# Performance work log

Measured on AMD Instinct MI355X. Metric: run time of the kernel, lower is better.

## Reference

```python
import jax, jax.numpy as jnp
import numpy as np

N_NODES = 100000
N_EDGES = 1600000
IN_DIM = 128
HID = 128
OUT_DIM = 64
EPS = 1e-8


def setup_inputs() -> dict:
    key = jax.random.key(0)
    ks = jax.random.split(key, 10)
    x = jax.random.normal(ks[0], (N_NODES, IN_DIM), dtype=jnp.float32)
    edge_index = jax.random.randint(ks[1], (2, N_EDGES), 0, N_NODES, dtype=jnp.int64)
    edge_attr = jax.random.uniform(ks[2], (N_EDGES, 4), dtype=jnp.float32)
    s1 = 1.0 / np.sqrt(IN_DIM)
    s2 = 1.0 / np.sqrt(HID)
    sr = 1.0 / np.sqrt(2 * HID)
    W1 = jax.random.normal(ks[3], (HID, IN_DIM), dtype=jnp.float32) * s1
    b1 = jnp.zeros((HID,), dtype=jnp.float32)
    W2 = jax.random.normal(ks[4], (HID, HID), dtype=jnp.float32) * s2
    b2 = jnp.zeros((HID,), dtype=jnp.float32)
    Wr = jax.random.normal(ks[5], (OUT_DIM, 2 * HID), dtype=jnp.float32) * sr
    br = jnp.zeros((OUT_DIM,), dtype=jnp.float32)
    return {"x": x, "edge_index": edge_index, "edge_attr": edge_attr,
            "W1": W1, "b1": b1, "W2": W2, "b2": b2, "Wr": Wr, "br": br}


def _edge_weight_from_attr_auto(edge_attr):
    # mean over features, min-max normalize, invert, clamp >= 0
    m = edge_attr.mean(axis=-1)                      # [E]
    m_min, m_max = m.min(), m.max()
    m_norm = (m - m_min) / (m_max - m_min + EPS)
    w = jnp.where(m_max - m_min > EPS, 1.0 - m_norm, jnp.ones_like(m))
    return jnp.clip(w, 0.0)


def reference(x, edge_index, edge_attr, W1, b1, W2, b2, Wr, br):
    N = x.shape[0]
    row, col = edge_index[0], edge_index[1]          # source -> target
    ew = _edge_weight_from_attr_auto(edge_attr)      # [E]
    # GCN normalization with self-loops (self-loop weight = 1.0)
    deg = jax.ops.segment_sum(ew, col, num_segments=N) + 1.0   # [N]
    dis = jax.lax.rsqrt(deg)                         # deg >= 1
    norm = dis[row] * ew * dis[col]                  # [E]

    def gcn(h, W, b):
        hW = h @ W.T                                 # [N, d_out]
        agg = jax.ops.segment_sum(norm[:, None] * hW[row], col, num_segments=N)
        # self-loop contribution: dis[i] * 1.0 * dis[i] * hW[i]
        return agg + (dis * dis)[:, None] * hW + b

    # dropout in eval mode -> identity
    h1 = jax.nn.relu(gcn(x, W1, b1))                 # [N, HID]
    h2 = jax.nn.relu(gcn(h1, W2, b2))                # [N, HID]
    hcat = jnp.concatenate([h1, h2], axis=-1)        # [N, 2*HID] (JK concat)
    return hcat @ Wr.T + br                          # residue-level [N, OUT_DIM]
```

## Files before the change

kernel.cpp:

```cpp
#include <hip/hip_runtime.h>

#define NN 100000
#define NE 1600000
#define HID 128
#define ODIM 64
#define NBK 196
#define BSHIFT 9
#define BGRID 800
#define CVTB 32
#define GEMMB 3125
#define CHUNK 2000
#define BITER 8
#define BINCAP 12288
#define SMAX 2588
#define LMAX 647

typedef unsigned int u32;
typedef unsigned short u16;
typedef __bf16 bf16x8 __attribute__((ext_vector_type(8)));
typedef float f32x4 __attribute__((ext_vector_type(4)));
typedef float f32x2 __attribute__((ext_vector_type(2)));

__device__ __forceinline__ float bf_lo(u32 p){ return __uint_as_float(p << 16); }
__device__ __forceinline__ float bf_hi(u32 p){ return __uint_as_float(p & 0xffff0000u); }
__device__ __forceinline__ u16 f2bf(float f){
  u32 u = __float_as_uint(f);
  u += 0x7fffu + ((u >> 16) & 1u);
  return (u16)(u >> 16);
}
__device__ __forceinline__ bf16x8 ld8bf(const u16* p){ return *(const bf16x8*)p; }
__device__ __forceinline__ bf16x8 cvt8(const float* p){
  union { bf16x8 v; u16 s[8]; } r;
#pragma unroll
  for (int i = 0; i < 8; i++) r.s[i] = f2bf(p[i]);
  return r.v;
}

__device__ __forceinline__ void wparams(const u32* minmax, float* A, float* B){
  u32 mnq = 32767u - minmax[0];
  u32 mxq = minmax[1];
  u32 rngq = mxq - mnq;
  float inv = rngq ? 1.f / ((float)rngq * (1.f / 32767.f) + 1e-8f) : 0.f;
  *A = 1.f + (float)mnq * (1.f / 32767.f) * inv;
  *B = inv * (1.f / 32767.f);
}

__global__ __launch_bounds__(256, 4) void k_front(
    const float* __restrict__ eattr, const int* __restrict__ erow,
    const int* __restrict__ ecol, u32* __restrict__ bcur,
    u32* __restrict__ binA, u16* __restrict__ binM, u32* __restrict__ minmax,
    const float* __restrict__ x, const float* __restrict__ W1,
    const float* __restrict__ W2, const float* __restrict__ Wr,
    u16* __restrict__ W2b, u16* __restrict__ Wrb, u16* __restrict__ graw){
  int tid = threadIdx.x;
  int bid = blockIdx.x;
  if (bid >= BGRID + CVTB){
    int gblk = bid - BGRID - CVTB;
    int wave = tid >> 6, lane = tid & 63;
    int m0 = gblk * 32;
    int m = lane & 15, q = lane >> 4;
    const float* a0f = x + (size_t)(m0 + m) * HID;
    const float* a1f = a0f + (size_t)16 * HID;
    const float* brow0 = W1 + (size_t)(wave * 16 + m) * HID;
    const float* brow1 = brow0 + (size_t)64 * HID;
    f32x4 acc00 = {0.f,0.f,0.f,0.f}, acc01 = {0.f,0.f,0.f,0.f};
    f32x4 acc10 = {0.f,0.f,0.f,0.f}, acc11 = {0.f,0.f,0.f,0.f};
#pragma unroll
    for (int kb = 0; kb < HID; kb += 32){
      bf16x8 af0 = cvt8(a0f + kb + q * 8);
      bf16x8 af1 = cvt8(a1f + kb + q * 8);
      bf16x8 bf0 = cvt8(brow0 + kb + q * 8);
      bf16x8 bf1 = cvt8(brow1 + kb + q * 8);
      acc00 = __builtin_amdgcn_mfma_f32_16x16x32_bf16(af0, bf0, acc00, 0, 0, 0);
      acc01 = __builtin_amdgcn_mfma_f32_16x16x32_bf16(af0, bf1, acc01, 0, 0, 0);
      acc10 = __builtin_amdgcn_mfma_f32_16x16x32_bf16(af1, bf0, acc10, 0, 0, 0);
      acc11 = __builtin_amdgcn_mfma_f32_16x16x32_bf16(af1, bf1, acc11, 0, 0, 0);
    }
    u16* crow0 = graw + (size_t)(m0 + q * 4) * HID + wave * 16 + m;
    u16* crow1 = crow0 + (size_t)16 * HID;
#pragma unroll
    for (int r = 0; r < 4; r++){
      crow0[(size_t)r * HID]      = f2bf(acc00[r]);
      crow0[(size_t)r * HID + 64] = f2bf(acc01[r]);
      crow1[(size_t)r * HID]      = f2bf(acc10[r]);
      crow1[(size_t)r * HID + 64] = f2bf(acc11[r]);
    }
    return;
  }
  if (bid >= BGRID){
    int i = (bid - BGRID) * 256 + tid;
    const float* src; u16* dst; int off;
    if (i < 4096){ src = W2; dst = W2b; off = i; }
    else { src = Wr; dst = Wrb; off = i - 4096; }
    float4 v = ((const float4*)src)[off];
    uint2 o;
    o.x = (u32)f2bf(v.x) | ((u32)f2bf(v.y) << 16);
    o.y = (u32)f2bf(v.z) | ((u32)f2bf(v.w) << 16);
    ((uint2*)dst)[off] = o;
    return;
  }
  __shared__ u32 lcnt4[4 * NBK], wof4[4 * NBK];
  __shared__ u32 lofs[NBK], gb[NBK];
  __shared__ u32 scn[256];
  __shared__ u16 lmap[LMAX];
  __shared__ u32 stageA[SMAX];
  __shared__ u16 stageM[SMAX];
  __shared__ u32 Tt;
  __shared__ u32 sMn[4], sMx[4];
  for (int t = tid; t < 4 * NBK; t += 256) lcnt4[t] = 0;
  __syncthreads();
  int base = bid * CHUNK;
  int wid = tid >> 6, lane = tid & 63;
  u32 lmn = 0, lmx = 0;
  u32 pk[BITER], sd[BITER], mq8[BITER];
#pragma unroll
  for (int it = 0; it < BITER; it++){
    int idx = it * 256 + tid;
    u32 p = 0xFFFFFFFFu, srcd = 0, mq = 0;
    if (idx < CHUNK){
      int e = base + idx;
      float4 a = ((const float4*)eattr)[e];
      float m = 0.25f * (a.x + a.y + a.z + a.w);
      mq = (u32)(m * 32767.f + 0.5f);
      lmn = max(lmn, 32767u - mq); lmx = max(lmx, mq);
      int c = ecol[e];
      u32 s = (u32)erow[e]; if (s >= NN) s = 0;
      if ((u32)c < NN){
        u32 b = (u32)c >> BSHIFT;
        u32 r = atomicAdd(&lcnt4[wid * NBK + b], 1u);
        p = (b << 21) | r;
        srcd = s | (((u32)c & 511u) << 17);
      }
    }
    pk[it] = p; sd[it] = srcd; mq8[it] = mq;
  }
  __syncthreads();
  u32 na = 0, n = 0;
  if (tid < NBK){
    u32 n0 = lcnt4[tid], n1 = lcnt4[NBK + tid];
    u32 n2 = lcnt4[2 * NBK + tid], n3 = lcnt4[3 * NBK + tid];
    n = n0 + n1 + n2 + n3;
    na = (n + 3u) & ~3u;
    wof4[tid] = 0; wof4[NBK + tid] = n0;
    wof4[2 * NBK + tid] = n0 + n1; wof4[3 * NBK + tid] = n0 + n1 + n2;
  }
  scn[tid] = na; __syncthreads();
  for (int s = 1; s < 256; s <<= 1){
    u32 t = (tid >= s) ? scn[tid - s] : 0;
    __syncthreads();
    scn[tid] += t;
    __syncthreads();
  }
  u32 ex = scn[tid] - na;
  if (tid < NBK){
    lofs[tid] = ex;
    u32 g = 0x80000000u;
    if (na){
      u32 gl = atomicAdd(&bcur[tid], na);
      if (gl + na <= BINCAP) g = (u32)tid * BINCAP + gl;
    }
    gb[tid] = g;
    for (u32 l = ex >> 2; l < (ex + na) >> 2; l++) lmap[l] = (u16)tid;
    for (u32 k = n; k < na; k++){ stageA[ex + k] = 0xFFFFFFFFu; stageM[ex + k] = 0; }
  }
  if (tid == 255) Tt = scn[255];
  __syncthreads();
#pragma unroll
  for (int it = 0; it < BITER; it++){
    u32 p = pk[it];
    if (p == 0xFFFFFFFFu) continue;
    u32 b = p >> 21;
    u32 slot = lofs[b] + wof4[wid * NBK + b] + (p & 4095u);
    stageA[slot] = sd[it];
    stageM[slot] = (u16)mq8[it];
  }
  __syncthreads();
  u32 T = Tt;
  for (u32 i = tid; i < T; i += 256){
    u32 b = lmap[i >> 2];
    u32 g = gb[b];
    if (g != 0x80000000u){
      u32 o = g + (i - lofs[b]);
      binA[o] = stageA[i];
      binM[o] = stageM[i];
    }
  }
  for (int off = 32; off; off >>= 1){
    lmn = max(lmn, (u32)__shfl_xor((int)lmn, off));
    lmx = max(lmx, (u32)__shfl_xor((int)lmx, off));
  }
  if (lane == 0){ sMn[wid] = lmn; sMx[wid] = lmx; }
  __syncthreads();
  if (tid == 0){
    u32 mn = max(max(sMn[0], sMn[1]), max(sMn[2], sMn[3]));
    u32 mx = max(max(sMx[0], sMx[1]), max(sMx[2], sMx[3]));
    atomicMax(&minmax[0], mn);
    atomicMax(&minmax[1], mx);
  }
}

__global__ __launch_bounds__(1024) void k_scatter(
    const u32* __restrict__ bcur, const u32* __restrict__ binA,
    const u16* __restrict__ binM, const u32* __restrict__ minmax,
    u32* __restrict__ csr, u32* __restrict__ meta, float* __restrict__ dis){
  __shared__ u32 cntL[512], sumL[512], curL[512];
  __shared__ u32 wtot[8];
  int b = blockIdx.x, tid = threadIdx.x;
  int bb = b * BINCAP;
  int nrec = (int)min(bcur[b], (u32)BINCAP);
  if (tid < 512){ cntL[tid] = 0; sumL[tid] = 0; }
  __syncthreads();
  for (int i = tid; i < nrec; i += 1024){
    u32 a = binA[bb + i];
    if (a == 0xFFFFFFFFu) continue;
    u32 d = (a >> 17) & 511u;
    u32 mq = binM[bb + i];
    atomicAdd(&cntL[d], 1u);
    atomicAdd(&sumL[d], mq);
  }
  __syncthreads();
  float A, B; wparams(minmax, &A, &B);
  int wid = tid >> 6, lane = tid & 63;
  u32 v = 0, incl = 0;
  if (tid < 512){ v = cntL[tid]; incl = v; }
  for (int off = 1; off < 64; off <<= 1){
    u32 t = (u32)__shfl_up((int)incl, off);
    if (lane >= off) incl += t;
  }
  if (tid < 512 && lane == 63) wtot[wid] = incl;
  __syncthreads();
  if (tid < 512){
    u32 pre = 0;
#pragma unroll
    for (int k = 0; k < 8; k++) pre += (k < wid) ? wtot[k] : 0u;
    u32 ex = pre + incl - v;
    curL[tid] = (u32)bb + ex;
    int node = (b << BSHIFT) + tid;
    if (node < NN){
      meta[node] = ((u32)bb + ex) | (v << 22);
      float sw = A * (float)v - B * (float)sumL[tid];
      dis[node] = rsqrtf(1.f + sw);
    }
  }
  __syncthreads();
  for (int i = tid; i < nrec; i += 1024){
    u32 a = binA[bb + i];
    if (a == 0xFFFFFFFFu) continue;
    u32 d = (a >> 17) & 511u;
    u32 mq = binM[bb + i];
    u32 pos = atomicAdd(&curL[d], 1u);
    csr[pos] = (a & 0x1FFFFu) | (mq << 17);
  }
}

__global__ __launch_bounds__(256) void k_gemm128(
    const u16* __restrict__ Ab, const u16* __restrict__ Bt,
    const float* __restrict__ dis, u16* __restrict__ G){
  int wave = threadIdx.x >> 6, lane = threadIdx.x & 63;
  int m0 = blockIdx.x * 32;
  int m = lane & 15, q = lane >> 4;
  const u16* a0b = Ab + (size_t)(m0 + m) * HID;
  const u16* a1b = a0b + (size_t)16 * HID;
  const u16* brow0 = Bt + (size_t)(wave * 16 + m) * HID;
  const u16* brow1 = brow0 + (size_t)64 * HID;
  f32x4 acc00 = {0.f,0.f,0.f,0.f}, acc01 = {0.f,0.f,0.f,0.f};
  f32x4 acc10 = {0.f,0.f,0.f,0.f}, acc11 = {0.f,0.f,0.f,0.f};
#pragma unroll
  for (int kb = 0; kb < HID; kb += 32){
    bf16x8 af0 = ld8bf(a0b + kb + q * 8);
    bf16x8 af1 = ld8bf(a1b + kb + q * 8);
    bf16x8 bf0 = ld8bf(brow0 + kb + q * 8);
    bf16x8 bf1 = ld8bf(brow1 + kb + q * 8);
    acc00 = __builtin_amdgcn_mfma_f32_16x16x32_bf16(af0, bf0, acc00, 0, 0, 0);
    acc01 = __builtin_amdgcn_mfma_f32_16x16x32_bf16(af0, bf1, acc01, 0, 0, 0);
    acc10 = __builtin_amdgcn_mfma_f32_16x16x32_bf16(af1, bf0, acc10, 0, 0, 0);
    acc11 = __builtin_amdgcn_mfma_f32_16x16x32_bf16(af1, bf1, acc11, 0, 0, 0);
  }
  u16* crow0 = G + (size_t)(m0 + q * 4) * HID + wave * 16 + m;
  u16* crow1 = crow0 + (size_t)16 * HID;
#pragma unroll
  for (int r = 0; r < 4; r++){
    float d0 = dis[m0 + q * 4 + r];
    float d1 = dis[m0 + 16 + q * 4 + r];
    crow0[(size_t)r * HID]      = f2bf(acc00[r] * d0);
    crow0[(size_t)r * HID + 64] = f2bf(acc01[r] * d0);
    crow1[(size_t)r * HID]      = f2bf(acc10[r] * d1);
    crow1[(size_t)r * HID + 64] = f2bf(acc11[r] * d1);
  }
}

template <bool FD>
__global__ __launch_bounds__(256) void k_aggregate(
    const u32* __restrict__ meta, const u32* __restrict__ csr,
    const float* __restrict__ dis, const u32* __restrict__ minmax,
    const u16* __restrict__ g, const float* __restrict__ bias,
    u16* __restrict__ hout){
  int node = __builtin_amdgcn_readfirstlane(
      (int)(blockIdx.x * 4 + (threadIdx.x >> 6)));
  int lane = threadIdx.x & 63;
  const u32* gp = (const u32*)g;
  u32 sv = gp[((size_t)node << 6) + lane];
  u32 mw = meta[node];
  float di = dis[node];
  float A, B; wparams(minmax, &A, &B);
  u32 s = mw & 0x3FFFFFu;
  int c = (int)(mw >> 22);
  const u32* cp = csr + s;
  f32x2 acc = {0.f, 0.f};
  int j = 0;
  for (; j + 16 <= c; j += 16){
    u32 p[16];
#pragma unroll
    for (int t = 0; t < 16; t++)
      p[t] = __builtin_amdgcn_readfirstlane(cp[j + t]);
    u32 pv[16];
#pragma unroll
    for (int t = 0; t < 16; t++)
      pv[t] = gp[(size_t)(p[t] & 0x1FFFFu) * 64u + lane];
#pragma unroll
    for (int t = 0; t < 16; t++){
      float wf = A - B * (float)(p[t] >> 17);
      if (FD) wf *= dis[p[t] & 0x1FFFFu];
      f32x2 val = {bf_lo(pv[t]), bf_hi(pv[t])};
      f32x2 w2 = {wf, wf};
      acc += w2 * val;
    }
  }
  for (; j < c; j += 8){
    u32 p[8];
#pragma unroll
    for (int t = 0; t < 8; t++)
      p[t] = __builtin_amdgcn_readfirstlane(cp[j + t]);
    u32 st[8]; float wv[8];
#pragma unroll
    for (int t = 0; t < 8; t++){
      bool ok = (j + t) < c;
      st[t] = ok ? (p[t] & 0x1FFFFu) : 0u;
      float wf = A - B * (float)(p[t] >> 17);
      if (FD) wf *= dis[st[t]];
      wv[t] = ok ? wf : 0.f;
    }
    u32 pv[8];
#pragma unroll
    for (int t = 0; t < 8; t++)
      pv[t] = gp[(size_t)st[t] * 64u + lane];
#pragma unroll
    for (int t = 0; t < 8; t++){
      f32x2 val = {bf_lo(pv[t]), bf_hi(pv[t])};
      f32x2 w2 = {wv[t], wv[t]};
      acc += w2 * val;
    }
  }
  float2 bv = ((const float2*)bias)[lane];
  f32x2 selfv = {bf_lo(sv), bf_hi(sv)};
  float sc = FD ? di : 1.f;
  float o0 = fmaxf((acc.x + sc * selfv.x) * di + bv.x, 0.f);
  float o1 = fmaxf((acc.y + sc * selfv.y) * di + bv.y, 0.f);
  ((u32*)hout)[((size_t)node << 6) + lane] = (u32)f2bf(o0) | ((u32)f2bf(o1) << 16);
}

__global__ __launch_bounds__(256) void k_readout(
    const u16* __restrict__ h1, const u16* __restrict__ h2,
    const u16* __restrict__ Wrb, const float* __restrict__ br, float* __restrict__ out){
  int wave = threadIdx.x >> 6, lane = threadIdx.x & 63;
  int m0 = blockIdx.x * 32;
  int n0 = wave * 16;
  int m = lane & 15, q = lane >> 4;
  const u16* a10 = h1 + (size_t)(m0 + m) * HID;
  const u16* a11 = a10 + (size_t)16 * HID;
  const u16* a20 = h2 + (size_t)(m0 + m) * HID;
  const u16* a21 = a20 + (size_t)16 * HID;
  const u16* b  = Wrb + (size_t)(n0 + m) * (2 * HID);
  f32x4 acc0 = {0.f,0.f,0.f,0.f}, acc1 = {0.f,0.f,0.f,0.f};
#pragma unroll
  for (int kb = 0; kb < HID; kb += 32){
    bf16x8 bf = ld8bf(b + kb + q * 8);
    acc0 = __builtin_amdgcn_mfma_f32_16x16x32_bf16(ld8bf(a10 + kb + q * 8), bf, acc0, 0, 0, 0);
    acc1 = __builtin_amdgcn_mfma_f32_16x16x32_bf16(ld8bf(a11 + kb + q * 8), bf, acc1, 0, 0, 0);
  }
#pragma unroll
  for (int kb = 0; kb < HID; kb += 32){
    bf16x8 bf = ld8bf(b + HID + kb + q * 8);
    acc0 = __builtin_amdgcn_mfma_f32_16x16x32_bf16(ld8bf(a20 + kb + q * 8), bf, acc0, 0, 0, 0);
    acc1 = __builtin_amdgcn_mfma_f32_16x16x32_bf16(ld8bf(a21 + kb + q * 8), bf, acc1, 0, 0, 0);
  }
  float bias = br[n0 + m];
  float* crow0 = out + (size_t)(m0 + q * 4) * ODIM + n0 + m;
  float* crow1 = crow0 + (size_t)16 * ODIM;
#pragma unroll
  for (int r = 0; r < 4; r++){
    crow0[(size_t)r * ODIM] = acc0[r] + bias;
    crow1[(size_t)r * ODIM] = acc1[r] + bias;
  }
}

extern "C" void kernel_launch(void* const* d_in, const int* in_sizes, int n_in,
                              void* d_out, int out_size, void* d_ws, size_t ws_size,
                              hipStream_t stream){
  const float* x     = (const float*)d_in[0];
  const int*   eidx  = (const int*)d_in[1];
  const float* eattr = (const float*)d_in[2];
  const float* W1    = (const float*)d_in[3];
  const float* b1    = (const float*)d_in[4];
  const float* W2    = (const float*)d_in[5];
  const float* b2    = (const float*)d_in[6];
  const float* Wr    = (const float*)d_in[7];
  const float* br    = (const float*)d_in[8];
  const int* erow  = eidx;
  const int* ecol  = eidx + NE;

  char* w = (char*)d_ws;
  auto carve = [&](size_t bytes) -> void* {
    void* p = (void*)w;
    w += (bytes + 255) & ~(size_t)255;
    return p;
  };
  u32* csr       = (u32*)carve((size_t)NBK * BINCAP * 4);
  u32* bcur      = (u32*)carve(1024);
  u32* minmax    = (u32*)carve(256);
  u32* meta      = (u32*)carve((size_t)NN * 4);
  float* dis     = (float*)carve((size_t)NN * 4);
  u16* W2b       = (u16*)carve((size_t)HID * HID * 2);
  u16* Wrb       = (u16*)carve((size_t)ODIM * 2 * HID * 2);
  u16* g         = (u16*)carve((size_t)NN * HID * 2);
  u16* h1        = (u16*)carve((size_t)NN * HID * 2);
  u16* h2        = (u16*)carve((size_t)NN * HID * 2);
  u32* binA      = (u32*)h2;
  u16* binM      = (u16*)((char*)h2 + (size_t)NBK * BINCAP * 4);

  hipMemsetAsync(bcur, 0, 1280, stream);
  k_front<<<BGRID + CVTB + GEMMB, 256, 0, stream>>>(
      eattr, erow, ecol, bcur, binA, binM, minmax,
      x, W1, W2, Wr, W2b, Wrb, g);
  k_scatter<<<NBK, 1024, 0, stream>>>(bcur, binA, binM, minmax, csr, meta, dis);
  k_aggregate<true><<<NN / 4, 256, 0, stream>>>(meta, csr, dis, minmax, g, b1, h1);
  k_gemm128<<<NN / 32, 256, 0, stream>>>(h1, W2b, dis, g);
  k_aggregate<false><<<NN / 4, 256, 0, stream>>>(meta, csr, dis, minmax, g, b2, h2);
  k_readout<<<NN / 32, 256, 0, stream>>>(h1, h2, Wrb, br, (float*)d_out);
}
```

Baseline: 390.5 us.

## Enlarge k_front blocks to 1024 threads and defer edge-attr loads to scatter phase

```diff
diff --git a/kernel.cpp b/kernel.cpp
--- a/kernel.cpp
+++ b/kernel.cpp
@@ -6,14 +6,14 @@
 #define ODIM 64
 #define NBK 196
 #define BSHIFT 9
-#define BGRID 800
-#define CVTB 32
-#define GEMMB 3125
-#define CHUNK 2000
+#define BINB 200
+#define CVTB 8
+#define GEMMB 782
+#define CHUNK 8000
 #define BITER 8
 #define BINCAP 12288
-#define SMAX 2588
-#define LMAX 647
+#define SMAX 8588
+#define LMAX 2148
 
 typedef unsigned int u32;
 typedef unsigned short u16;
@@ -45,7 +45,7 @@
   *B = inv * (1.f / 32767.f);
 }
 
-__global__ __launch_bounds__(256, 4) void k_front(
+__global__ __launch_bounds__(1024, 8) void k_front(
     const float* __restrict__ eattr, const int* __restrict__ erow,
     const int* __restrict__ ecol, u32* __restrict__ bcur,
     u32* __restrict__ binA, u16* __restrict__ binM, u32* __restrict__ minmax,
@@ -54,14 +54,15 @@
     u16* __restrict__ W2b, u16* __restrict__ Wrb, u16* __restrict__ graw){
   int tid = threadIdx.x;
   int bid = blockIdx.x;
-  if (bid >= BGRID + CVTB){
-    int gblk = bid - BGRID - CVTB;
-    int wave = tid >> 6, lane = tid & 63;
-    int m0 = gblk * 32;
+  if (bid >= BINB + CVTB){
+    int gblk = bid - BINB - CVTB;
+    int wv = tid >> 6, lane = tid & 63;
+    int mg = wv >> 2, ng = wv & 3;
+    int m0 = gblk * 128 + mg * 32;
     int m = lane & 15, q = lane >> 4;
-    const float* a0f = x + (size_t)(m0 + m) * HID;
-    const float* a1f = a0f + (size_t)16 * HID;
-    const float* brow0 = W1 + (size_t)(wave * 16 + m) * HID;
+    const float* a0f = x + (size_t)min(m0 + m, NN - 1) * HID;
+    const float* a1f = x + (size_t)min(m0 + 16 + m, NN - 1) * HID;
+    const float* brow0 = W1 + (size_t)(ng * 16 + m) * HID;
     const float* brow1 = brow0 + (size_t)64 * HID;
     f32x4 acc00 = {0.f,0.f,0.f,0.f}, acc01 = {0.f,0.f,0.f,0.f};
     f32x4 acc10 = {0.f,0.f,0.f,0.f}, acc11 = {0.f,0.f,0.f,0.f};
@@ -76,19 +77,24 @@
       acc10 = __builtin_amdgcn_mfma_f32_16x16x32_bf16(af1, bf0, acc10, 0, 0, 0);
       acc11 = __builtin_amdgcn_mfma_f32_16x16x32_bf16(af1, bf1, acc11, 0, 0, 0);
     }
-    u16* crow0 = graw + (size_t)(m0 + q * 4) * HID + wave * 16 + m;
-    u16* crow1 = crow0 + (size_t)16 * HID;
 #pragma unroll
     for (int r = 0; r < 4; r++){
-      crow0[(size_t)r * HID]      = f2bf(acc00[r]);
-      crow0[(size_t)r * HID + 64] = f2bf(acc01[r]);
-      crow1[(size_t)r * HID]      = f2bf(acc10[r]);
-      crow1[(size_t)r * HID + 64] = f2bf(acc11[r]);
+      int row0 = m0 + q * 4 + r, row1 = m0 + 16 + q * 4 + r;
+      if (row0 < NN){
+        u16* c0 = graw + (size_t)row0 * HID + ng * 16 + m;
+        c0[0]  = f2bf(acc00[r]);
+        c0[64] = f2bf(acc01[r]);
+      }
+      if (row1 < NN){
+        u16* c1 = graw + (size_t)row1 * HID + ng * 16 + m;
+        c1[0]  = f2bf(acc10[r]);
+        c1[64] = f2bf(acc11[r]);
+      }
     }
     return;
   }
-  if (bid >= BGRID){
-    int i = (bid - BGRID) * 256 + tid;
+  if (bid >= BINB){
+    int i = (bid - BINB) * 1024 + tid;
     const float* src; u16* dst; int off;
     if (i < 4096){ src = W2; dst = W2b; off = i; }
     else { src = Wr; dst = Wrb; off = i - 4096; }
@@ -99,84 +105,96 @@
     ((uint2*)dst)[off] = o;
     return;
   }
-  __shared__ u32 lcnt4[4 * NBK], wof4[4 * NBK];
+  __shared__ u32 lcnt[8 * NBK], wof[8 * NBK];
   __shared__ u32 lofs[NBK], gb[NBK];
-  __shared__ u32 scn[256];
+  __shared__ u32 wtot[4];
   __shared__ u16 lmap[LMAX];
   __shared__ u32 stageA[SMAX];
   __shared__ u16 stageM[SMAX];
   __shared__ u32 Tt;
-  __shared__ u32 sMn[4], sMx[4];
-  for (int t = tid; t < 4 * NBK; t += 256) lcnt4[t] = 0;
+  __shared__ u32 sMn[16], sMx[16];
+  for (int t = tid; t < 8 * NBK; t += 1024) lcnt[t] = 0;
   __syncthreads();
   int base = bid * CHUNK;
-  int wid = tid >> 6, lane = tid & 63;
-  u32 lmn = 0, lmx = 0;
-  u32 pk[BITER], sd[BITER], mq8[BITER];
+  int wv = tid >> 6, lane = tid & 63;
+  int grp = tid >> 7;
+  u32 pk[BITER];
 #pragma unroll
   for (int it = 0; it < BITER; it++){
-    int idx = it * 256 + tid;
-    u32 p = 0xFFFFFFFFu, srcd = 0, mq = 0;
+    int idx = it * 1024 + tid;
+    u32 p = 0xFFFFFFFFu;
     if (idx < CHUNK){
-      int e = base + idx;
-      float4 a = ((const float4*)eattr)[e];
-      float m = 0.25f * (a.x + a.y + a.z + a.w);
-      mq = (u32)(m * 32767.f + 0.5f);
-      lmn = max(lmn, 32767u - mq); lmx = max(lmx, mq);
-      int c = ecol[e];
-      u32 s = (u32)erow[e]; if (s >= NN) s = 0;
+      int c = ecol[base + idx];
       if ((u32)c < NN){
         u32 b = (u32)c >> BSHIFT;
-        u32 r = atomicAdd(&lcnt4[wid * NBK + b], 1u);
-        p = (b << 21) | r;
-        srcd = s | (((u32)c & 511u) << 17);
+        u32 r = atomicAdd(&lcnt[grp * NBK + b], 1u);
+        p = (b << 22) | (((u32)c & 511u) << 13) | r;
       }
     }
-    pk[it] = p; sd[it] = srcd; mq8[it] = mq;
-  }
-  __syncthreads();
-  u32 na = 0, n = 0;
+    pk[it] = p;
+  }
+  __syncthreads();
+  u32 na = 0;
   if (tid < NBK){
-    u32 n0 = lcnt4[tid], n1 = lcnt4[NBK + tid];
-    u32 n2 = lcnt4[2 * NBK + tid], n3 = lcnt4[3 * NBK + tid];
-    n = n0 + n1 + n2 + n3;
-    na = (n + 3u) & ~3u;
-    wof4[tid] = 0; wof4[NBK + tid] = n0;
-    wof4[2 * NBK + tid] = n0 + n1; wof4[3 * NBK + tid] = n0 + n1 + n2;
-  }
-  scn[tid] = na; __syncthreads();
-  for (int s = 1; s < 256; s <<= 1){
-    u32 t = (tid >= s) ? scn[tid - s] : 0;
-    __syncthreads();
-    scn[tid] += t;
-    __syncthreads();
-  }
-  u32 ex = scn[tid] - na;
-  if (tid < NBK){
-    lofs[tid] = ex;
-    u32 g = 0x80000000u;
-    if (na){
-      u32 gl = atomicAdd(&bcur[tid], na);
-      if (gl + na <= BINCAP) g = (u32)tid * BINCAP + gl;
-    }
-    gb[tid] = g;
-    for (u32 l = ex >> 2; l < (ex + na) >> 2; l++) lmap[l] = (u16)tid;
-    for (u32 k = n; k < na; k++){ stageA[ex + k] = 0xFFFFFFFFu; stageM[ex + k] = 0; }
-  }
-  if (tid == 255) Tt = scn[255];
-  __syncthreads();
+    u32 run = 0;
+#pragma unroll
+    for (int g = 0; g < 8; g++){
+      wof[g * NBK + tid] = run;
+      run += lcnt[g * NBK + tid];
+    }
+    na = (run + 3u) & ~3u;
+    lofs[tid] = run;
+  }
+  u32 incl = na;
+  if (tid < 256){
+    for (int off = 1; off < 64; off <<= 1){
+      u32 t = (u32)__shfl_up((int)incl, off);
+      if (lane >= off) incl += t;
+    }
+    if (lane == 63) wtot[wv] = incl;
+  }
+  __syncthreads();
+  if (tid < 256){
+    u32 pre = 0;
+#pragma unroll
+    for (int k = 0; k < 4; k++) pre += (k < wv) ? wtot[k] : 0u;
+    u32 ex = pre + incl - na;
+    if (tid == 255) Tt = pre + incl;
+    if (tid < NBK){
+      u32 n = lofs[tid];
+      lofs[tid] = ex;
+      u32 g = 0x80000000u;
+      if (na){
+        u32 gl = atomicAdd(&bcur[tid], na);
+        if (gl + na <= BINCAP) g = (u32)tid * BINCAP + gl;
+      }
+      gb[tid] = g;
+      for (u32 l = ex >> 2; l < (ex + na) >> 2; l++) lmap[l] = (u16)tid;
+      for (u32 k = n; k < na; k++){ stageA[ex + k] = 0xFFFFFFFFu; stageM[ex + k] = 0; }
+    }
+  }
+  __syncthreads();
+  u32 lmn = 0, lmx = 0;
 #pragma unroll
   for (int it = 0; it < BITER; it++){
+    int idx = it * 1024 + tid;
+    if (idx >= CHUNK) continue;
+    int e = base + idx;
+    float4 a = ((const float4*)eattr)[e];
+    float m = 0.25f * (a.x + a.y + a.z + a.w);
+    u32 mq = (u32)(m * 32767.f + 0.5f);
+    lmn = max(lmn, 32767u - mq); lmx = max(lmx, mq);
     u32 p = pk[it];
     if (p == 0xFFFFFFFFu) continue;
-    u32 b = p >> 21;
-    u32 slot = lofs[b] + wof4[wid * NBK + b] + (p & 4095u);
-    stageA[slot] = sd[it];
-    stageM[slot] = (u16)mq8[it];
+    u32 s = (u32)erow[e]; if (s >= NN) s = 0;
+    u32 b = p >> 22, d = (p >> 13) & 511u, r = p & 8191u;
+    u32 slot = lofs[b] + wof[grp * NBK + b] + r;
+    stageA[slot] = s | (d << 17);
+    stageM[slot] = (u16)mq;
   }
   __syncthreads();
   u32 T = Tt;
-  for (u32 i = tid; i < T; i += 256){
+  for (u32 i = tid; i < T; i += 1024){
     u32 b = lmap[i >> 2];
     u32 g = gb[b];
     if (g != 0x80000000u){
@@ -189,11 +207,12 @@
     lmn = max(lmn, (u32)__shfl_xor((int)lmn, off));
     lmx = max(lmx, (u32)__shfl_xor((int)lmx, off));
   }
-  if (lane == 0){ sMn[wid] = lmn; sMx[wid] = lmx; }
+  if (lane == 0){ sMn[wv] = lmn; sMx[wv] = lmx; }
   __syncthreads();
   if (tid == 0){
-    u32 mn = max(max(sMn[0], sMn[1]), max(sMn[2], sMn[3]));
-    u32 mx = max(max(sMx[0], sMx[1]), max(sMx[2], sMx[3]));
+    u32 mn = 0, mx = 0;
+#pragma unroll
+    for (int k = 0; k < 16; k++){ mn = max(mn, sMn[k]); mx = max(mx, sMx[k]); }
     atomicMax(&minmax[0], mn);
     atomicMax(&minmax[1], mx);
   }
@@ -429,7 +448,7 @@
   u16* binM      = (u16*)((char*)h2 + (size_t)NBK * BINCAP * 4);
 
   hipMemsetAsync(bcur, 0, 1280, stream);
-  k_front<<<BGRID + CVTB + GEMMB, 256, 0, stream>>>(
+  k_front<<<BINB + CVTB + GEMMB, 1024, 0, stream>>>(
       eattr, erow, ecol, bcur, binA, binM, minmax,
       x, W1, W2, Wr, W2b, Wrb, g);
   k_scatter<<<NBK, 1024, 0, stream>>>(bcur, binA, binM, minmax, csr, meta, dis);
```

New measurement: 374.3 us. -4.1%, faster.
